# Optimization experiments

Hardware: AMD Instinct MI355X
Metric: run time of the kernel (lower is better)

The kernel has to match this reference:

```python
import jax, jax.numpy as jnp
import numpy as np

B, N, D = 8, 512, 3


def setup_inputs() -> dict:
    key = jax.random.key(0)
    ks = jax.random.split(key, 9)
    s = lambda fan_in: 1.0 / np.sqrt(fan_in)
    return {
        "coords": jax.random.normal(ks[0], (B, N, D), jnp.float32),
        "fw0": jax.random.normal(ks[1], (3, 64), jnp.float32) * s(3),
        "fb0": jnp.zeros((64,), jnp.float32),
        "fw1": jax.random.normal(ks[2], (64, 128), jnp.float32) * s(64),
        "fb1": jnp.zeros((128,), jnp.float32),
        "aw0": jax.random.normal(ks[3], (6, 64), jnp.float32) * s(6),
        "ab0": jnp.zeros((64,), jnp.float32),
        "aw1": jax.random.normal(ks[4], (64, 64), jnp.float32) * s(64),
        "ab1": jnp.zeros((64,), jnp.float32),
        "aw2": jax.random.normal(ks[5], (64, 1), jnp.float32) * s(64),
        "ab2": jnp.zeros((1,), jnp.float32),
        "uw0": jax.random.normal(ks[6], (259, 256), jnp.float32) * s(259),
        "ub0": jnp.zeros((256,), jnp.float32),
        "uw1": jax.random.normal(ks[7], (256, 128), jnp.float32) * s(256),
        "ub1": jnp.zeros((128,), jnp.float32),
    }


def reference(coords, fw0, fb0, fw1, fb1, aw0, ab0, aw1, ab1, aw2, ab2,
              uw0, ub0, uw1, ub1):
    relu = jax.nn.relu
    # node feature MLP: (B, N, 3) -> (B, N, 128)
    h = relu(relu(coords @ fw0 + fb0) @ fw1 + fb1)
    # pairwise concat: (B, N, N, 2D)
    nP = coords.shape[1]
    pi = jnp.broadcast_to(coords[:, :, None, :], (B, nP, nP, D))
    pj = jnp.broadcast_to(coords[:, None, :, :], (B, nP, nP, D))
    pair = jnp.concatenate([pi, pj], axis=-1)
    # adjacency MLP -> scalar per pair; note final layer also has relu
    a = relu(pair @ aw0 + ab0)
    a = relu(a @ aw1 + ab1)
    A = relu(a @ aw2 + ab2)[..., 0]  # (B, N, N)
    # aggregate
    V = jnp.matmul(A, h)  # (B, N, 128)
    updates = jnp.concatenate([h, coords, V], axis=-1)  # (B, N, 259)
    h_next = relu(relu(updates @ uw0 + ub0) @ uw1 + ub1)
    # max pool over points
    return jnp.max(h_next, axis=1)  # (B, 128)
```

## Files before the change

kernel.cpp:

```cpp
#include <hip/hip_runtime.h>
#include <hip/hip_bf16.h>

#define B_ 8
#define N_ 512

typedef __attribute__((ext_vector_type(8))) __bf16 bf16x8;
typedef __attribute__((ext_vector_type(8))) _Float16 f16x8;
typedef __attribute__((ext_vector_type(4))) _Float16 f16x4;
typedef __attribute__((ext_vector_type(2))) _Float16 h2;
typedef __attribute__((ext_vector_type(4))) float f32x4;
typedef __attribute__((ext_vector_type(4))) unsigned int u32x4;
typedef __attribute__((ext_vector_type(2))) unsigned int u32x2;

__device__ __forceinline__ unsigned pk_bf16(float hi, float lo) {
    return __builtin_amdgcn_perm(__builtin_bit_cast(unsigned, hi),
                                 __builtin_bit_cast(unsigned, lo), 0x07060302u);
}

__device__ __forceinline__ h2 pkrtz(float a, float b) {
    return __builtin_bit_cast(h2, __builtin_amdgcn_cvt_pkrtz(a, b));
}
__device__ __forceinline__ unsigned pkrtz_u(float a, float b) {
    return __builtin_bit_cast(unsigned, __builtin_amdgcn_cvt_pkrtz(a, b));
}
__device__ __forceinline__ unsigned relu2_u(h2 v) {
    const h2 z2 = {(_Float16)0.0f, (_Float16)0.0f};
    return __builtin_bit_cast(unsigned, __builtin_elementwise_max(v, z2));
}

__global__ __launch_bounds__(256) void k_prep(
    const float* __restrict__ coords,
    const float* __restrict__ fw0, const float* __restrict__ fb0,
    const float* __restrict__ fw1, const float* __restrict__ fb1,
    const float* __restrict__ uw0, const float* __restrict__ uw1,
    __bf16* __restrict__ h_bf, __bf16* __restrict__ h_t,
    __bf16* __restrict__ w0t, __bf16* __restrict__ w1t,
    float* __restrict__ out, int out_size)
{
    const int blk = blockIdx.x;
    const int t = threadIdx.x;

    if (blk < 1024) {
        const int row0 = blk << 2;
        const int b = row0 >> 9;
        const int n0 = row0 & 511;
        __shared__ float cds4[4][4];
        __shared__ float hid4[4][64];
        if (t < 12) {
            int r = t / 3, d = t - 3 * r;
            cds4[r][d] = coords[(size_t)row0 * 3 + t];
        }
        __syncthreads();
        {
            int r = t >> 6, ch = t & 63;
            float v = fb0[ch];
            v += cds4[r][0] * fw0[0 * 64 + ch];
            v += cds4[r][1] * fw0[1 * 64 + ch];
            v += cds4[r][2] * fw0[2 * 64 + ch];
            hid4[r][ch] = fmaxf(v, 0.0f);
        }
        __syncthreads();
        {
            int ch = t & 127;
            int rp = (t >> 7) << 1;
            float hv0 = fb1[ch], hv1 = hv0;
#pragma unroll 4
            for (int k = 0; k < 64; ++k) {
                float w = fw1[k * 128 + ch];
                hv0 += hid4[rp][k] * w;
                hv1 += hid4[rp + 1][k] * w;
            }
            hv0 = fmaxf(hv0, 0.0f);
            hv1 = fmaxf(hv1, 0.0f);
            h_bf[((size_t)(row0 + rp) << 7) + ch] = (__bf16)hv0;
            h_bf[((size_t)(row0 + rp + 1) << 7) + ch] = (__bf16)hv1;
            *(unsigned*)(h_t + (size_t)(b * 128 + ch) * 512 + n0 + rp) =
                pk_bf16(hv1, hv0);
        }
    } else if (blk < 1280) {
        int k = blk - 1024;
        int c = t;
        int src = (k < 128) ? k : (k + 3);
        w0t[(size_t)c * 256 + k] = (__bf16)uw0[(size_t)src * 256 + c];
    } else if (blk < 1408) {
        int id = (blk - 1280) * 256 + t;
        int c = id & 127, k = id >> 7;
        w1t[(size_t)c * 256 + k] = (__bf16)uw1[(size_t)k * 128 + c];
    } else {
        int i = (blk - 1408) * 256 + t;
        if (i < out_size) out[i] = 0.0f;
    }
}

#define AP 520
__global__ __launch_bounds__(1024) void k_fused(
    const float* __restrict__ coords,
    const float* __restrict__ aw0, const float* __restrict__ ab0,
    const float* __restrict__ aw1, const float* __restrict__ ab1,
    const float* __restrict__ aw2, const float* __restrict__ ab2,
    const __bf16* __restrict__ h_t, const __bf16* __restrict__ h_bf,
    const float* __restrict__ uw0, const float* __restrict__ ub0,
    const __bf16* __restrict__ w0t, const __bf16* __restrict__ w1t,
    const float* __restrict__ ub1,
    float* __restrict__ out)
{
    const int t = threadIdx.x;
    const int w = t >> 6;
    const int l = t & 63;
    const int q = l >> 4;
    const int m = l & 15;
    const int row0 = blockIdx.x << 4;
    const int b = row0 >> 9;

    __shared__ __align__(16) _Float16 s_aw1p[4096];
    __shared__ __align__(16) float s_w[576];
    __shared__ __align__(8) unsigned s_cj[512][2];
    __shared__ __align__(16) __bf16 As[16][AP];
    __shared__ __align__(16) __bf16 act[16][264];
    __shared__ __align__(16) __bf16 u1[16][264];
    __shared__ float vp[2][16][128];
    __shared__ float cds[16][4];

    {
        f32x4 wv = *(const f32x4*)(aw1 + t * 4);
        const int R = t >> 4;
        const int C4 = (t & 15) << 2;
        const int s = R >> 5, qq = (R >> 3) & 3, j = R & 7;
        const int ct = C4 >> 4, mm0 = C4 & 15;
        const int base = s * 2048 + ct * 512 + qq * 128 + mm0 * 8 + j;
#pragma unroll
        for (int e = 0; e < 4; ++e)
            s_aw1p[base + e * 8] = (_Float16)wv[e];

        if (t < 144) {
            const int o = t * 4;
            f32x4 v;
            if (o < 384)      v = *(const f32x4*)(aw0 + o);
            else if (o < 448) v = *(const f32x4*)(ab0 + (o - 384));
            else if (o < 512) v = *(const f32x4*)(aw2 + (o - 448));
            else              v = *(const f32x4*)(ab1 + (o - 512));
            *(f32x4*)&s_w[o] = v;
        }

        if (t < 512) {
            const float* cj = coords + ((size_t)b * N_ + t) * 3;
            s_cj[t][0] = pkrtz_u(cj[0], cj[1]);
            s_cj[t][1] = pkrtz_u(cj[2], 1.0f);
        }

        unsigned hv = *(const unsigned*)(h_bf + ((size_t)row0 << 7) + t * 2);
        *(unsigned*)&act[(t * 2) >> 7][(t * 2) & 127] = hv;

        if (t < 48) {
            int r = t / 3, d = t - 3 * r;
            cds[r][d] = coords[(size_t)row0 * 3 + t];
        }
    }
    __syncthreads();

    {
        const float* cp = coords + (size_t)(row0 + w) * 3;
        const float ci0 = cp[0], ci1 = cp[1], ci2 = cp[2];

        f16x4 a0f[4];
        {
            const int chb = ((m >> 2) << 3) + (m & 3);
            const int offs[4] = {0, 4, 32, 36};
#pragma unroll
            for (int t4 = 0; t4 < 4; ++t4) {
                const int ch = chb + offs[t4];
                float o = s_w[384 + ch] + ci0 * s_w[ch] + ci1 * s_w[64 + ch]
                                        + ci2 * s_w[128 + ch];
                u32x2 fr;
                fr[0] = (q == 0) ? pkrtz_u(s_w[192 + ch], s_w[256 + ch]) : 0u;
                fr[1] = (q == 0) ? pkrtz_u(s_w[320 + ch], o) : 0u;
                a0f[t4] = __builtin_bit_cast(f16x4, fr);
            }
        }

        f16x8 ewf[2];
#pragma unroll
        for (int g = 0; g < 2; ++g) {
            const float* e0 = &s_w[448 + g * 32 + (q << 2)];
            const float* e1 = e0 + 16;
            u32x4 fr;
            fr[0] = pkrtz_u(e0[0], e0[1]);
            fr[1] = pkrtz_u(e0[2], e0[3]);
            fr[2] = pkrtz_u(e1[0], e1[1]);
            fr[3] = pkrtz_u(e1[2], e1[3]);
            ewf[g] = __builtin_bit_cast(f16x8, fr);
        }

        f16x8 bfr[2][4];
#pragma unroll
        for (int s = 0; s < 2; ++s)
#pragma unroll
            for (int ct = 0; ct < 4; ++ct)
                bfr[s][ct] = *(const f16x8*)&s_aw1p[s * 2048 + ct * 512 + q * 128 + m * 8];

        f32x4 ab1q[4];
#pragma unroll
        for (int ct = 0; ct < 4; ++ct)
            ab1q[ct] = *(const f32x4*)&s_w[512 + ct * 16 + (q << 2)];

        const float ab2s = ab2[0];
        const f32x4 pr0 = {ab2s, ab2s, ab2s, ab2s};
        const f32x4 zf = {0.f, 0.f, 0.f, 0.f};

#pragma unroll 1
        for (int tt = 0; tt < 32; ++tt) {
            f16x4 bj = __builtin_bit_cast(f16x4, *(const u32x2*)s_cj[(tt << 4) + m]);

            f32x4 d0 = __builtin_amdgcn_mfma_f32_16x16x16f16(a0f[0], bj, zf, 0, 0, 0);
            f32x4 d1 = __builtin_amdgcn_mfma_f32_16x16x16f16(a0f[1], bj, zf, 0, 0, 0);
            f32x4 d2 = __builtin_amdgcn_mfma_f32_16x16x16f16(a0f[2], bj, zf, 0, 0, 0);
            f32x4 d3 = __builtin_amdgcn_mfma_f32_16x16x16f16(a0f[3], bj, zf, 0, 0, 0);

            u32x4 pa, pb;
            pa[0] = relu2_u(pkrtz(d0[0], d0[1]));
            pa[1] = relu2_u(pkrtz(d0[2], d0[3]));
            pa[2] = relu2_u(pkrtz(d1[0], d1[1]));
            pa[3] = relu2_u(pkrtz(d1[2], d1[3]));
            pb[0] = relu2_u(pkrtz(d2[0], d2[1]));
            pb[1] = relu2_u(pkrtz(d2[2], d2[3]));
            pb[2] = relu2_u(pkrtz(d3[0], d3[1]));
            pb[3] = relu2_u(pkrtz(d3[2], d3[3]));
            f16x8 a0 = __builtin_bit_cast(f16x8, pa);
            f16x8 a1 = __builtin_bit_cast(f16x8, pb);

            f32x4 c0v = __builtin_amdgcn_mfma_f32_16x16x32_f16(bfr[0][0], a0, ab1q[0], 0, 0, 0);
            c0v = __builtin_amdgcn_mfma_f32_16x16x32_f16(bfr[1][0], a1, c0v, 0, 0, 0);
            f32x4 c1v = __builtin_amdgcn_mfma_f32_16x16x32_f16(bfr[0][1], a0, ab1q[1], 0, 0, 0);
            c1v = __builtin_amdgcn_mfma_f32_16x16x32_f16(bfr[1][1], a1, c1v, 0, 0, 0);
            f32x4 c2v = __builtin_amdgcn_mfma_f32_16x16x32_f16(bfr[0][2], a0, ab1q[2], 0, 0, 0);
            c2v = __builtin_amdgcn_mfma_f32_16x16x32_f16(bfr[1][2], a1, c2v, 0, 0, 0);
            f32x4 c3v = __builtin_amdgcn_mfma_f32_16x16x32_f16(bfr[0][3], a0, ab1q[3], 0, 0, 0);
            c3v = __builtin_amdgcn_mfma_f32_16x16x32_f16(bfr[1][3], a1, c3v, 0, 0, 0);

            u32x4 B0, B1;
            B0[0] = relu2_u(pkrtz(c0v[0], c0v[1]));
            B0[1] = relu2_u(pkrtz(c0v[2], c0v[3]));
            B0[2] = relu2_u(pkrtz(c1v[0], c1v[1]));
            B0[3] = relu2_u(pkrtz(c1v[2], c1v[3]));
            B1[0] = relu2_u(pkrtz(c2v[0], c2v[1]));
            B1[1] = relu2_u(pkrtz(c2v[2], c2v[3]));
            B1[2] = relu2_u(pkrtz(c3v[0], c3v[1]));
            B1[3] = relu2_u(pkrtz(c3v[2], c3v[3]));

            f32x4 pr = __builtin_amdgcn_mfma_f32_16x16x32_f16(
                ewf[0], __builtin_bit_cast(f16x8, B0), pr0, 0, 0, 0);
            pr = __builtin_amdgcn_mfma_f32_16x16x32_f16(
                ewf[1], __builtin_bit_cast(f16x8, B1), pr, 0, 0, 0);

            if (l < 16) As[w][(tt << 4) + l] = (__bf16)fmaxf(pr[0], 0.0f);
        }
    }
    __syncthreads();

    const int gw = w & 7;
    const int ks = w >> 3;
    {
        const __bf16* hp = h_t + ((size_t)b << 16) + (size_t)(gw * 16 + m) * 512
                           + ks * 256 + q * 8;
        const __bf16* Ar = &As[m][ks * 256 + q * 8];
        f32x4 acc = {0.f, 0.f, 0.f, 0.f};
#pragma unroll 4
        for (int kt = 0; kt < 8; ++kt) {
            bf16x8 av = *(const bf16x8*)(Ar + kt * 32);
            bf16x8 bv = *(const bf16x8*)(hp + kt * 32);
            acc = __builtin_amdgcn_mfma_f32_16x16x32_bf16(av, bv, acc, 0, 0, 0);
        }
#pragma unroll
        for (int r = 0; r < 4; ++r)
            vp[ks][q * 4 + r][gw * 16 + m] = acc[r];
    }
    __syncthreads();

#pragma unroll
    for (int it = 0; it < 2; ++it) {
        int idx = t + it * 1024;
        int row = idx >> 7, ch = idx & 127;
        act[row][128 + ch] = (__bf16)(vp[0][row][ch] + vp[1][row][ch]);
    }
    __syncthreads();

    bf16x8 af[8];
#pragma unroll
    for (int ch = 0; ch < 8; ++ch)
        af[ch] = *(const bf16x8*)&act[m][q * 8 + 32 * ch];
    {
        const int c = w * 16 + m;
        const float wx = uw0[128 * 256 + c];
        const float wy = uw0[129 * 256 + c];
        const float wz = uw0[130 * 256 + c];
        const float bias = ub0[c];
        f32x4 a1c;
#pragma unroll
        for (int r = 0; r < 4; ++r)
            a1c[r] = bias + cds[q * 4 + r][0] * wx + cds[q * 4 + r][1] * wy
                          + cds[q * 4 + r][2] * wz;
        const __bf16* wp = w0t + (size_t)c * 256 + q * 8;
#pragma unroll
        for (int ch = 0; ch < 8; ++ch) {
            bf16x8 bfr = *(const bf16x8*)(wp + 32 * ch);
            a1c = __builtin_amdgcn_mfma_f32_16x16x32_bf16(af[ch], bfr, a1c, 0, 0, 0);
        }
#pragma unroll
        for (int r = 0; r < 4; ++r)
            u1[q * 4 + r][c] = (__bf16)fmaxf(a1c[r], 0.0f);
    }
    __syncthreads();

    if (w < 8) {
        bf16x8 af2[8];
#pragma unroll
        for (int ch = 0; ch < 8; ++ch)
            af2[ch] = *(const bf16x8*)&u1[m][q * 8 + 32 * ch];
        const int c = w * 16 + m;
        float bias = ub1[c];
        f32x4 a2c = {bias, bias, bias, bias};
        const __bf16* wp = w1t + (size_t)c * 256 + q * 8;
#pragma unroll
        for (int ch = 0; ch < 8; ++ch) {
            bf16x8 bfr = *(const bf16x8*)(wp + 32 * ch);
            a2c = __builtin_amdgcn_mfma_f32_16x16x32_bf16(af2[ch], bfr, a2c, 0, 0, 0);
        }
        float mx = fmaxf(fmaxf(a2c[0], a2c[1]), fmaxf(a2c[2], a2c[3]));
        mx = fmaxf(mx, 0.0f);
        mx = fmaxf(mx, __shfl_xor(mx, 16, 64));
        mx = fmaxf(mx, __shfl_xor(mx, 32, 64));
        if (l < 16)
            atomicMax((int*)(out + ((size_t)b << 7) + c), __float_as_int(mx));
    }
}

extern "C" void kernel_launch(void* const* d_in, const int* in_sizes, int n_in,
                              void* d_out, int out_size, void* d_ws, size_t ws_size,
                              hipStream_t stream)
{
    const float* coords = (const float*)d_in[0];
    const float* fw0 = (const float*)d_in[1];
    const float* fb0 = (const float*)d_in[2];
    const float* fw1 = (const float*)d_in[3];
    const float* fb1 = (const float*)d_in[4];
    const float* aw0 = (const float*)d_in[5];
    const float* ab0 = (const float*)d_in[6];
    const float* aw1 = (const float*)d_in[7];
    const float* ab1 = (const float*)d_in[8];
    const float* aw2 = (const float*)d_in[9];
    const float* ab2 = (const float*)d_in[10];
    const float* uw0 = (const float*)d_in[11];
    const float* ub0 = (const float*)d_in[12];
    const float* uw1 = (const float*)d_in[13];
    const float* ub1 = (const float*)d_in[14];
    float* out = (float*)d_out;

    char* ws = (char*)d_ws;
    __bf16* h_t  = (__bf16*)(ws);
    __bf16* h_bf = (__bf16*)(ws + (1u << 20));
    __bf16* w0t  = (__bf16*)(ws + (2u << 20));
    __bf16* w1t  = (__bf16*)(ws + (2u << 20) + (128u << 10));

    k_prep<<<1412, 256, 0, stream>>>(coords, fw0, fb0, fw1, fb1, uw0, uw1,
                                     h_bf, h_t, w0t, w1t, out, out_size);
    k_fused<<<256, 1024, 0, stream>>>(coords, aw0, ab0, aw1, ab1, aw2, ab2,
                                      h_t, h_bf, uw0, ub0, w0t, w1t, ub1, out);
}
```

Before: 122.4 us.

## Halve rows per block and split pairwise columns across two waves

Each block now handles 8 query rows instead of 16, and two waves share each row by splitting the 512 neighbor columns in half. The grid doubles to 512 blocks so all 256 CUs get two blocks, addressing poor CU occupancy with only 256 blocks. The trade-off is that the later MFMA stages run at half utilization: 16-row tiles are filled with duplicated rows and half the results are discarded. Per-block setup such as weight staging into LDS is also repeated twice as often.

```diff
diff --git a/kernel.cpp b/kernel.cpp
--- a/kernel.cpp
+++ b/kernel.cpp
@@ -109,17 +109,17 @@
     const int l = t & 63;
     const int q = l >> 4;
     const int m = l & 15;
-    const int row0 = blockIdx.x << 4;
+    const int row0 = blockIdx.x << 3;
     const int b = row0 >> 9;
 
     __shared__ __align__(16) _Float16 s_aw1p[4096];
     __shared__ __align__(16) float s_w[576];
     __shared__ __align__(8) unsigned s_cj[512][2];
-    __shared__ __align__(16) __bf16 As[16][AP];
-    __shared__ __align__(16) __bf16 act[16][264];
-    __shared__ __align__(16) __bf16 u1[16][264];
-    __shared__ float vp[2][16][128];
-    __shared__ float cds[16][4];
+    __shared__ __align__(16) __bf16 As[8][AP];
+    __shared__ __align__(16) __bf16 act[8][264];
+    __shared__ __align__(16) __bf16 u1[8][264];
+    __shared__ float vp[2][8][128];
+    __shared__ float cds[8][4];
 
     {
         f32x4 wv = *(const f32x4*)(aw1 + t * 4);
@@ -146,12 +146,12 @@
             const float* cj = coords + ((size_t)b * N_ + t) * 3;
             s_cj[t][0] = pkrtz_u(cj[0], cj[1]);
             s_cj[t][1] = pkrtz_u(cj[2], 1.0f);
-        }
-
-        unsigned hv = *(const unsigned*)(h_bf + ((size_t)row0 << 7) + t * 2);
-        *(unsigned*)&act[(t * 2) >> 7][(t * 2) & 127] = hv;
-
-        if (t < 48) {
+
+            unsigned hv = *(const unsigned*)(h_bf + ((size_t)row0 << 7) + t * 2);
+            *(unsigned*)&act[(t * 2) >> 7][(t * 2) & 127] = hv;
+        }
+
+        if (t < 24) {
             int r = t / 3, d = t - 3 * r;
             cds[r][d] = coords[(size_t)row0 * 3 + t];
         }
@@ -159,7 +159,9 @@
     __syncthreads();
 
     {
-        const float* cp = coords + (size_t)(row0 + w) * 3;
+        const int r8 = w >> 1;
+        const int jh = w & 1;
+        const float* cp = coords + (size_t)(row0 + r8) * 3;
         const float ci0 = cp[0], ci1 = cp[1], ci2 = cp[2];
 
         f16x4 a0f[4];
@@ -208,8 +210,9 @@
         const f32x4 zf = {0.f, 0.f, 0.f, 0.f};
 
 #pragma unroll 1
-        for (int tt = 0; tt < 32; ++tt) {
-            f16x4 bj = __builtin_bit_cast(f16x4, *(const u32x2*)s_cj[(tt << 4) + m]);
+        for (int tt = 0; tt < 16; ++tt) {
+            f16x4 bj = __builtin_bit_cast(
+                f16x4, *(const u32x2*)s_cj[jh * 256 + (tt << 4) + m]);
 
             f32x4 d0 = __builtin_amdgcn_mfma_f32_16x16x16f16(a0f[0], bj, zf, 0, 0, 0);
             f32x4 d1 = __builtin_amdgcn_mfma_f32_16x16x16f16(a0f[1], bj, zf, 0, 0, 0);
@@ -252,7 +255,8 @@
             pr = __builtin_amdgcn_mfma_f32_16x16x32_f16(
                 ewf[1], __builtin_bit_cast(f16x8, B1), pr, 0, 0, 0);
 
-            if (l < 16) As[w][(tt << 4) + l] = (__bf16)fmaxf(pr[0], 0.0f);
+            if (l < 16)
+                As[r8][jh * 256 + (tt << 4) + l] = (__bf16)fmaxf(pr[0], 0.0f);
         }
     }
     __syncthreads();
@@ -262,7 +266,7 @@
     {
         const __bf16* hp = h_t + ((size_t)b << 16) + (size_t)(gw * 16 + m) * 512
                            + ks * 256 + q * 8;
-        const __bf16* Ar = &As[m][ks * 256 + q * 8];
+        const __bf16* Ar = &As[m & 7][ks * 256 + q * 8];
         f32x4 acc = {0.f, 0.f, 0.f, 0.f};
 #pragma unroll 4
         for (int kt = 0; kt < 8; ++kt) {
@@ -270,16 +274,16 @@
             bf16x8 bv = *(const bf16x8*)(hp + kt * 32);
             acc = __builtin_amdgcn_mfma_f32_16x16x32_bf16(av, bv, acc, 0, 0, 0);
         }
-#pragma unroll
-        for (int r = 0; r < 4; ++r)
-            vp[ks][q * 4 + r][gw * 16 + m] = acc[r];
-    }
-    __syncthreads();
-
-#pragma unroll
-    for (int it = 0; it < 2; ++it) {
-        int idx = t + it * 1024;
-        int row = idx >> 7, ch = idx & 127;
+        if (q < 2) {
+#pragma unroll
+            for (int r = 0; r < 4; ++r)
+                vp[ks][q * 4 + r][gw * 16 + m] = acc[r];
+        }
+    }
+    __syncthreads();
+
+    {
+        int row = t >> 7, ch = t & 127;
         act[row][128 + ch] = (__bf16)(vp[0][row][ch] + vp[1][row][ch]);
     }
     __syncthreads();
@@ -287,7 +291,7 @@
     bf16x8 af[8];
 #pragma unroll
     for (int ch = 0; ch < 8; ++ch)
-        af[ch] = *(const bf16x8*)&act[m][q * 8 + 32 * ch];
+        af[ch] = *(const bf16x8*)&act[m & 7][q * 8 + 32 * ch];
     {
         const int c = w * 16 + m;
         const float wx = uw0[128 * 256 + c];
@@ -297,17 +301,20 @@
         f32x4 a1c;
 #pragma unroll
         for (int r = 0; r < 4; ++r)
-            a1c[r] = bias + cds[q * 4 + r][0] * wx + cds[q * 4 + r][1] * wy
-                          + cds[q * 4 + r][2] * wz;
+            a1c[r] = bias + cds[(q * 4 + r) & 7][0] * wx
+                          + cds[(q * 4 + r) & 7][1] * wy
+                          + cds[(q * 4 + r) & 7][2] * wz;
         const __bf16* wp = w0t + (size_t)c * 256 + q * 8;
 #pragma unroll
         for (int ch = 0; ch < 8; ++ch) {
             bf16x8 bfr = *(const bf16x8*)(wp + 32 * ch);
             a1c = __builtin_amdgcn_mfma_f32_16x16x32_bf16(af[ch], bfr, a1c, 0, 0, 0);
         }
-#pragma unroll
-        for (int r = 0; r < 4; ++r)
-            u1[q * 4 + r][c] = (__bf16)fmaxf(a1c[r], 0.0f);
+        if (q < 2) {
+#pragma unroll
+            for (int r = 0; r < 4; ++r)
+                u1[q * 4 + r][c] = (__bf16)fmaxf(a1c[r], 0.0f);
+        }
     }
     __syncthreads();
 
@@ -315,7 +322,7 @@
         bf16x8 af2[8];
 #pragma unroll
         for (int ch = 0; ch < 8; ++ch)
-            af2[ch] = *(const bf16x8*)&u1[m][q * 8 + 32 * ch];
+            af2[ch] = *(const bf16x8*)&u1[m & 7][q * 8 + 32 * ch];
         const int c = w * 16 + m;
         float bias = ub1[c];
         f32x4 a2c = {bias, bias, bias, bias};
@@ -363,6 +370,6 @@
 
     k_prep<<<1412, 256, 0, stream>>>(coords, fw0, fb0, fw1, fb1, uw0, uw1,
                                      h_bf, h_t, w0t, w1t, out, out_size);
-    k_fused<<<256, 1024, 0, stream>>>(coords, aw0, ab0, aw1, ab1, aw2, ab2,
+    k_fused<<<512, 1024, 0, stream>>>(coords, aw0, ab0, aw1, ab1, aw2, ab2,
                                       h_t, h_bf, uw0, ub0, w0t, w1t, ub1, out);
 }
```

Result: slower. 133.9 us (+9.4%).
